# Optimization experiments

Hardware: AMD Instinct MI355X
Metric: run time of the kernel (lower is better)

Reference implementation:

```python
import jax, jax.numpy as jnp
import numpy as np

BETA = 0.25  # commitment cost
EPS = 1e-10


def _vq_layer(part, cb):
    # part: [B, C, H, W], cb: [K, C]
    B, C, H, W = part.shape
    K = cb.shape[0]
    flat = part.transpose(0, 2, 3, 1).reshape(-1, C)  # [N, C]
    d2 = (jnp.sum(flat * flat, axis=1, keepdims=True)
          - 2.0 * flat @ cb.T
          + jnp.sum(cb * cb, axis=1))  # [N, K]
    idx = jnp.argmin(d2, axis=1)  # [N]
    quant = cb[idx].reshape(B, H, W, C).transpose(0, 3, 1, 2)  # [B, C, H, W]
    e_latent = jnp.mean((jax.lax.stop_gradient(quant) - part) ** 2)
    q_latent = jnp.mean((quant - jax.lax.stop_gradient(part)) ** 2)
    loss = q_latent + BETA * e_latent  # scalar
    # straight-through estimator
    quant_st = part + jax.lax.stop_gradient(quant - part)
    # perplexity (codebook usage)
    counts = jnp.zeros((K,), dtype=part.dtype).at[idx].add(1.0)
    avg_probs = counts / idx.shape[0]
    perplexity = jnp.exp(-jnp.sum(avg_probs * jnp.log(avg_probs + EPS)))
    return quant_st, idx.reshape(B, H, W), loss, perplexity


def setup_inputs() -> dict:
    key = jax.random.key(0)
    ks = jax.random.split(key, 5)
    x = jax.random.normal(ks[0], (16, 256, 64, 64), dtype=jnp.float32)
    out = {"x": x}
    for i in range(4):
        out[f"codebook{i}"] = jax.random.normal(ks[i + 1], (1024, 64), dtype=jnp.float32)
    return out


def reference(x, codebook0, codebook1, codebook2, codebook3):
    dim_list = [64, 64, 64, 64]
    codebooks = [codebook0, codebook1, codebook2, codebook3]
    quants, indices, losses, perps = [], [], [], []
    start = 0
    for i in range(4):
        part = x[:, start:start + dim_list[i], :, :]
        start += dim_list[i]
        q, idx, loss, perp = _vq_layer(part, codebooks[i])
        quants.append(q)
        indices.append(idx)
        losses.append(loss)
        perps.append(perp)
    quantized_cat = jnp.concatenate(quants, axis=1)          # [B, 256, H, W]
    indices_cat = jnp.stack(indices, axis=1)                  # [B, 4, H, W]
    loss_cat = jnp.stack(losses, axis=0)                      # [4]
    perplexity_cat = jnp.stack(perps, axis=0)                 # [4]
    return quantized_cat, indices_cat, loss_cat, perplexity_cat
```

## Files before the change

kernel.cpp:

```cpp
#include <hip/hip_runtime.h>
#include <math.h>

#define HW 4096
#define CH 64
#define NCODE 1024
#define TAU 0.05f
#define FLAGCAP 65536u

#define OUT_IDX  16777216
#define OUT_LOSS 17039360
#define OUT_PERP 17039364

#define WS_C2    0
#define WS_CNT   4096
#define WS_SUM   8192
#define WS_FLAGC 8196
#define WS_FLAGL 8208
#define WS_CBP   73744

typedef short bf16x8 __attribute__((ext_vector_type(8)));
typedef float f32x4v __attribute__((ext_vector_type(4)));

static __device__ __forceinline__ unsigned f2u(float f) { return __float_as_uint(f); }
static __device__ __forceinline__ float u2f(unsigned u) { return __uint_as_float(u); }
static __device__ __forceinline__ unsigned short bf16rne(float f) {
  unsigned u = f2u(f);
  unsigned r = u + 0x7FFFu + ((u >> 16) & 1u);
  return (unsigned short)(r >> 16);
}

__global__ __launch_bounds__(256) void vq_prep(const float* __restrict__ cb0, const float* __restrict__ cb1,
                                               const float* __restrict__ cb2, const float* __restrict__ cb3,
                                               float* __restrict__ ws) {
  int gid = blockIdx.x * 256 + threadIdx.x;
  int l = gid >> 10, code = gid & 1023;
  const float* cbs[4] = {cb0, cb1, cb2, cb3};
  const float* row = cbs[l] + (size_t)code * CH;

  unsigned short* cbpack = (unsigned short*)(ws + WS_CBP);
  const int kt = code >> 5, m = (code >> 4) & 1, rowc = code & 15;
  const size_t base = (size_t)l * 131072 + (size_t)kt * 4096;

  float c2 = 0.f;
#pragma unroll 8
  for (int c = 0; c < CH; ++c) {
    float v = row[c];
    c2 = fmaf(v, v, c2);
    float aa = -2.f * v;
    unsigned short ah = bf16rne(aa);
    float rest = aa - u2f((unsigned)ah << 16);
    unsigned short al = bf16rne(rest);
    int s0 = c, s1 = 64 + c;
    cbpack[base + (size_t)(m * 4 + (s0 >> 5)) * 512 + (size_t)(((s0 >> 3) & 3) * 16 + rowc) * 8 + (s0 & 7)] = ah;
    cbpack[base + (size_t)(m * 4 + (s1 >> 5)) * 512 + (size_t)(((s1 >> 3) & 3) * 16 + rowc) * 8 + (s1 & 7)] = al;
  }
  ws[WS_C2 + gid] = c2;
  ws[WS_CNT + gid] = 0.f;
  if (gid < 4) ws[WS_SUM + gid] = 0.f;
  if (gid == 0) *((unsigned*)(ws + WS_FLAGC)) = 0u;
}

__global__ __launch_bounds__(256, 2) void vq_argmin(
    const float* __restrict__ x, float* __restrict__ ws, float* __restrict__ out) {
  const int layer = blockIdx.y;
  const int wid = threadIdx.x >> 6;
  const int lane = threadIdx.x & 63;
  const int rowl = lane & 15, g = lane >> 4;

  const int p0 = blockIdx.x * 256 + wid * 64;
  const int b = p0 >> 12;
  const int hwb = (p0 & 4095) + rowl;
  const float* xb = x + (size_t)(b * 256 + layer * 64) * HW;

  bf16x8 xf[4][4];
#pragma unroll
  for (int n = 0; n < 4; ++n) {
    int hw = hwb + n * 16;
#pragma unroll
    for (int j = 0; j < 8; ++j) {
      float v0 = xb[(size_t)(g * 8 + j) * HW + hw];
      float v1 = xb[(size_t)(32 + g * 8 + j) * HW + hw];
      unsigned short h0 = bf16rne(v0);
      unsigned short h1 = bf16rne(v1);
      float r0 = v0 - u2f((unsigned)h0 << 16);
      float r1 = v1 - u2f((unsigned)h1 << 16);
      xf[n][0][j] = (short)h0;
      xf[n][1][j] = (short)h1;
      xf[n][2][j] = (short)bf16rne(r0);
      xf[n][3][j] = (short)bf16rne(r1);
    }
  }

  const unsigned short* cbl = (const unsigned short*)(ws + WS_CBP) + (size_t)layer * 131072;
  const float* c2l = ws + WS_C2 + layer * NCODE;

  float d1[4], d2[4];
  int k1[4];
#pragma unroll
  for (int n = 0; n < 4; ++n) { d1[n] = 1e30f; d2[n] = 1e30f; k1[n] = 0; }

  for (int kt = 0; kt < 32; ++kt) {
    const unsigned short* cbase = cbl + (size_t)kt * 4096 + lane * 8;
#pragma unroll
    for (int m = 0; m < 2; ++m) {
      bf16x8 ch0 = *(const bf16x8*)(cbase + (m * 4 + 0) * 512);
      bf16x8 ch1 = *(const bf16x8*)(cbase + (m * 4 + 1) * 512);
      bf16x8 cl0 = *(const bf16x8*)(cbase + (m * 4 + 2) * 512);
      bf16x8 cl1 = *(const bf16x8*)(cbase + (m * 4 + 3) * 512);
      f32x4v c2v = *(const f32x4v*)(c2l + kt * 32 + m * 16 + g * 4);
      const int kb = kt * 32 + m * 16 + g * 4;
#pragma unroll
      for (int n = 0; n < 4; ++n) {
        f32x4v a = {0.f, 0.f, 0.f, 0.f};
        a = __builtin_amdgcn_mfma_f32_16x16x32_bf16(ch0, xf[n][0], a, 0, 0, 0);
        a = __builtin_amdgcn_mfma_f32_16x16x32_bf16(ch1, xf[n][1], a, 0, 0, 0);
        a = __builtin_amdgcn_mfma_f32_16x16x32_bf16(cl0, xf[n][0], a, 0, 0, 0);
        a = __builtin_amdgcn_mfma_f32_16x16x32_bf16(cl1, xf[n][1], a, 0, 0, 0);
        a = __builtin_amdgcn_mfma_f32_16x16x32_bf16(ch0, xf[n][2], a, 0, 0, 0);
        a = __builtin_amdgcn_mfma_f32_16x16x32_bf16(ch1, xf[n][3], a, 0, 0, 0);
#pragma unroll
        for (int r = 0; r < 4; ++r) {
          float d = a[r] + c2v[r];
          bool lt = d < d1[n];
          d2[n] = fminf(d2[n], fmaxf(d, d1[n]));
          d1[n] = fminf(d1[n], d);
          k1[n] = lt ? (kb + r) : k1[n];
        }
      }
    }
  }

  unsigned* flagcnt = (unsigned*)(ws + WS_FLAGC);
  unsigned* flaglist = (unsigned*)(ws + WS_FLAGL);
#pragma unroll
  for (int n = 0; n < 4; ++n) {
    float e1 = d1[n], e2 = d2[n];
    int ek = k1[n];
#pragma unroll
    for (int off = 16; off <= 32; off <<= 1) {
      float o1 = __shfl_xor(e1, off);
      float o2 = __shfl_xor(e2, off);
      int ok = __shfl_xor(ek, off);
      bool take = (o1 < e1) || (o1 == e1 && ok < ek);
      float loser = take ? e1 : o1;
      e2 = fminf(fminf(e2, o2), loser);
      e1 = take ? o1 : e1;
      ek = take ? ok : ek;
    }
    if (g == 0) {
      int p = p0 + n * 16 + rowl;
      int hw = p & 4095;
      size_t orow = (size_t)(b * 4 + layer) * HW + hw;
      out[OUT_IDX + orow] = (float)ek;
      if (e2 - e1 < TAU) {
        unsigned pos = atomicAdd(flagcnt, 1u);
        if (pos < FLAGCAP) flaglist[pos] = (unsigned)orow;
      }
    }
  }
}

__global__ __launch_bounds__(64) void vq_refine(
    const float* __restrict__ x,
    const float* __restrict__ cb0, const float* __restrict__ cb1,
    const float* __restrict__ cb2, const float* __restrict__ cb3,
    const float* __restrict__ ws, float* __restrict__ out) {
  unsigned count = *((const unsigned*)(ws + WS_FLAGC));
  if (count > FLAGCAP) count = FLAGCAP;
  const unsigned* flaglist = (const unsigned*)(ws + WS_FLAGL);

  for (unsigned i = blockIdx.x; i < count; i += gridDim.x) {
    unsigned r = flaglist[i];
    int l = (r >> 12) & 3;
    int bb = r >> 14;
    int hw = r & 4095;
    const float* cb = (l == 0) ? cb0 : (l == 1) ? cb1 : (l == 2) ? cb2 : cb3;
    const float* xb = x + (size_t)(bb * 256 + l * 64) * HW + hw;
    double f[CH];
#pragma unroll
    for (int c = 0; c < CH; ++c) f[c] = (double)xb[(size_t)c * HW];
    double bd = 1e300;
    int bk = 0;
    for (int j = 0; j < 16; ++j) {
      int k = threadIdx.x + j * 64;
      const float* cr = cb + (size_t)k * CH;
      double dot = 0.0, cc = 0.0;
#pragma unroll
      for (int c = 0; c < CH; ++c) {
        double cv = (double)cr[c];
        cc = fma(cv, cv, cc);
        dot = fma(f[c], cv, dot);
      }
      double d = cc - 2.0 * dot;
      if (d < bd || (d == bd && k < bk)) { bd = d; bk = k; }
    }
    for (int off = 1; off < 64; off <<= 1) {
      double od = __shfl_xor(bd, off);
      int ok = __shfl_xor(bk, off);
      if (od < bd || (od == bd && ok < bk)) { bd = od; bk = ok; }
    }
    if (threadIdx.x == 0) out[OUT_IDX + r] = (float)bk;
  }
}

__global__ __launch_bounds__(256) void vq_gather(
    const float* __restrict__ x,
    const float* __restrict__ cb0, const float* __restrict__ cb1,
    const float* __restrict__ cb2, const float* __restrict__ cb3,
    float* __restrict__ out, float* __restrict__ ws) {
  __shared__ unsigned hist[NCODE];
  __shared__ float red[256];
  const int layer = blockIdx.y;
  const int t = threadIdx.x;
  const float* cb = (layer == 0) ? cb0 : (layer == 1) ? cb1 : (layer == 2) ? cb2 : cb3;

  for (int i = t; i < NCODE; i += 256) hist[i] = 0u;
  __syncthreads();

  const int pbase = blockIdx.x * 2048;
  int kk[8];
#pragma unroll
  for (int i = 0; i < 8; ++i) {
    int p = pbase + i * 256 + t;
    int bb = p >> 12, hw = p & 4095;
    int k = (int)out[OUT_IDX + (size_t)(bb * 4 + layer) * HW + hw];
    kk[i] = k;
    atomicAdd(&hist[k], 1u);
  }

  float ls = 0.f;
#pragma unroll
  for (int i = 0; i < 8; ++i) {
    int p = pbase + i * 256 + t;
    int bb = p >> 12, hw = p & 4095;
    const float* xp = x + (size_t)(bb * 256 + layer * 64) * HW + hw;
    float* qp = out + (size_t)(bb * 256 + layer * 64) * HW + hw;
    const float* cr = cb + (size_t)kk[i] * CH;
#pragma unroll
    for (int c4 = 0; c4 < 16; ++c4) {
      float4 cv = *(const float4*)(cr + c4 * 4);
      float q[4] = {cv.x, cv.y, cv.z, cv.w};
#pragma unroll
      for (int j = 0; j < 4; ++j) {
        int c = c4 * 4 + j;
        float xv = xp[(size_t)c * HW];
        qp[(size_t)c * HW] = q[j];
        float dd = q[j] - xv;
        ls = fmaf(dd, dd, ls);
      }
    }
  }

  red[t] = ls;
  __syncthreads();
  for (int s = 128; s > 0; s >>= 1) {
    if (t < s) red[t] += red[t + s];
    __syncthreads();
  }
  if (t == 0) atomicAdd(&ws[WS_SUM + layer], red[0]);

  for (int i = t; i < NCODE; i += 256) {
    unsigned h = hist[i];
    if (h) atomicAdd(&ws[WS_CNT + layer * NCODE + i], (float)h);
  }
}

__global__ __launch_bounds__(256) void vq_final(const float* __restrict__ ws, float* __restrict__ out) {
  const int l = blockIdx.x;
  float h = 0.f;
#pragma unroll
  for (int j = 0; j < 4; ++j) {
    float cnt = ws[WS_CNT + l * NCODE + threadIdx.x + j * 256];
    float pr = cnt * (1.f / 65536.f);
    h += pr * logf(pr + 1e-10f);
  }
  __shared__ float red[256];
  red[threadIdx.x] = h;
  __syncthreads();
  for (int s = 128; s > 0; s >>= 1) {
    if (threadIdx.x < s) red[threadIdx.x] += red[threadIdx.x + s];
    __syncthreads();
  }
  if (threadIdx.x == 0) {
    out[OUT_LOSS + l] = 1.25f * ws[WS_SUM + l] / 4194304.f;
    out[OUT_PERP + l] = expf(-red[0]);
  }
}

extern "C" void kernel_launch(void* const* d_in, const int* in_sizes, int n_in,
                              void* d_out, int out_size, void* d_ws, size_t ws_size,
                              hipStream_t stream) {
  const float* x = (const float*)d_in[0];
  const float* cb0 = (const float*)d_in[1];
  const float* cb1 = (const float*)d_in[2];
  const float* cb2 = (const float*)d_in[3];
  const float* cb3 = (const float*)d_in[4];
  float* out = (float*)d_out;
  float* ws = (float*)d_ws;

  vq_prep  <<<dim3(16),     dim3(256), 0, stream>>>(cb0, cb1, cb2, cb3, ws);
  vq_argmin<<<dim3(256, 4), dim3(256), 0, stream>>>(x, ws, out);
  vq_refine<<<dim3(2048),   dim3(64),  0, stream>>>(x, cb0, cb1, cb2, cb3, ws, out);
  vq_gather<<<dim3(32, 4),  dim3(256), 0, stream>>>(x, cb0, cb1, cb2, cb3, out, ws);
  vq_final <<<dim3(4),      dim3(256), 0, stream>>>(ws, out);
}
```

Baseline: 352.7 us.

## Pack code index into distance bits, compute loss in argmin, slim gather

The argmin kernel now folds ||x||^2 and ||c||^2 into the MFMA accumulator init. It packs the code index into the low mantissa bits so the min/second-min tracking uses only fminf and med3, and it double-buffers codebook register loads across halves. The commitment loss is taken directly from the minimum distance, and refine corrects it when it changes an index, using precomputed double-precision code norms. The gather kernel no longer rereads x, so it only writes quantized values and the histogram. Truncating 10 mantissa bits lowers distance precision, and the flag threshold was made relative to compensate, which could flag more near-ties and raise refine work.

```diff
diff --git a/kernel.cpp b/kernel.cpp
--- a/kernel.cpp
+++ b/kernel.cpp
@@ -4,7 +4,6 @@
 #define HW 4096
 #define CH 64
 #define NCODE 1024
-#define TAU 0.05f
 #define FLAGCAP 65536u
 
 #define OUT_IDX  16777216
@@ -15,8 +14,9 @@
 #define WS_CNT   4096
 #define WS_SUM   8192
 #define WS_FLAGC 8196
-#define WS_FLAGL 8208
-#define WS_CBP   73744
+#define WS_C2D   8200
+#define WS_FLAGL 16392
+#define WS_CBP   81936
 
 typedef short bf16x8 __attribute__((ext_vector_type(8)));
 typedef float f32x4v __attribute__((ext_vector_type(4)));
@@ -42,10 +42,12 @@
   const size_t base = (size_t)l * 131072 + (size_t)kt * 4096;
 
   float c2 = 0.f;
+  double c2d = 0.0;
 #pragma unroll 8
   for (int c = 0; c < CH; ++c) {
     float v = row[c];
     c2 = fmaf(v, v, c2);
+    c2d = fma((double)v, (double)v, c2d);
     float aa = -2.f * v;
     unsigned short ah = bf16rne(aa);
     float rest = aa - u2f((unsigned)ah << 16);
@@ -55,31 +57,36 @@
     cbpack[base + (size_t)(m * 4 + (s1 >> 5)) * 512 + (size_t)(((s1 >> 3) & 3) * 16 + rowc) * 8 + (s1 & 7)] = al;
   }
   ws[WS_C2 + gid] = c2;
+  ((double*)(ws + WS_C2D))[gid] = c2d;
   ws[WS_CNT + gid] = 0.f;
   if (gid < 4) ws[WS_SUM + gid] = 0.f;
   if (gid == 0) *((unsigned*)(ws + WS_FLAGC)) = 0u;
 }
 
-__global__ __launch_bounds__(256, 2) void vq_argmin(
+__global__ __launch_bounds__(64, 4) void vq_argmin(
     const float* __restrict__ x, float* __restrict__ ws, float* __restrict__ out) {
   const int layer = blockIdx.y;
-  const int wid = threadIdx.x >> 6;
-  const int lane = threadIdx.x & 63;
+  const int lane = threadIdx.x;
   const int rowl = lane & 15, g = lane >> 4;
-
-  const int p0 = blockIdx.x * 256 + wid * 64;
+  const int g4 = g * 4;
+
+  const int p0 = blockIdx.x * 64;
   const int b = p0 >> 12;
   const int hwb = (p0 & 4095) + rowl;
   const float* xb = x + (size_t)(b * 256 + layer * 64) * HW;
 
   bf16x8 xf[4][4];
+  float x2[4];
 #pragma unroll
   for (int n = 0; n < 4; ++n) {
     int hw = hwb + n * 16;
+    float s = 0.f;
 #pragma unroll
     for (int j = 0; j < 8; ++j) {
       float v0 = xb[(size_t)(g * 8 + j) * HW + hw];
       float v1 = xb[(size_t)(32 + g * 8 + j) * HW + hw];
+      s = fmaf(v0, v0, s);
+      s = fmaf(v1, v1, s);
       unsigned short h0 = bf16rne(v0);
       unsigned short h1 = bf16rne(v1);
       float r0 = v0 - u2f((unsigned)h0 << 16);
@@ -89,85 +96,118 @@
       xf[n][2][j] = (short)bf16rne(r0);
       xf[n][3][j] = (short)bf16rne(r1);
     }
+    s += __shfl_xor(s, 16);
+    s += __shfl_xor(s, 32);
+    x2[n] = s;
   }
 
   const unsigned short* cbl = (const unsigned short*)(ws + WS_CBP) + (size_t)layer * 131072;
   const float* c2l = ws + WS_C2 + layer * NCODE;
 
   float d1[4], d2[4];
-  int k1[4];
-#pragma unroll
-  for (int n = 0; n < 4; ++n) { d1[n] = 1e30f; d2[n] = 1e30f; k1[n] = 0; }
-
-  for (int kt = 0; kt < 32; ++kt) {
-    const unsigned short* cbase = cbl + (size_t)kt * 4096 + lane * 8;
-#pragma unroll
-    for (int m = 0; m < 2; ++m) {
-      bf16x8 ch0 = *(const bf16x8*)(cbase + (m * 4 + 0) * 512);
-      bf16x8 ch1 = *(const bf16x8*)(cbase + (m * 4 + 1) * 512);
-      bf16x8 cl0 = *(const bf16x8*)(cbase + (m * 4 + 2) * 512);
-      bf16x8 cl1 = *(const bf16x8*)(cbase + (m * 4 + 3) * 512);
-      f32x4v c2v = *(const f32x4v*)(c2l + kt * 32 + m * 16 + g * 4);
-      const int kb = kt * 32 + m * 16 + g * 4;
-#pragma unroll
-      for (int n = 0; n < 4; ++n) {
-        f32x4v a = {0.f, 0.f, 0.f, 0.f};
-        a = __builtin_amdgcn_mfma_f32_16x16x32_bf16(ch0, xf[n][0], a, 0, 0, 0);
-        a = __builtin_amdgcn_mfma_f32_16x16x32_bf16(ch1, xf[n][1], a, 0, 0, 0);
-        a = __builtin_amdgcn_mfma_f32_16x16x32_bf16(cl0, xf[n][0], a, 0, 0, 0);
-        a = __builtin_amdgcn_mfma_f32_16x16x32_bf16(cl1, xf[n][1], a, 0, 0, 0);
-        a = __builtin_amdgcn_mfma_f32_16x16x32_bf16(ch0, xf[n][2], a, 0, 0, 0);
-        a = __builtin_amdgcn_mfma_f32_16x16x32_bf16(ch1, xf[n][3], a, 0, 0, 0);
-#pragma unroll
-        for (int r = 0; r < 4; ++r) {
-          float d = a[r] + c2v[r];
-          bool lt = d < d1[n];
-          d2[n] = fminf(d2[n], fmaxf(d, d1[n]));
-          d1[n] = fminf(d1[n], d);
-          k1[n] = lt ? (kb + r) : k1[n];
-        }
+#pragma unroll
+  for (int n = 0; n < 4; ++n) { d1[n] = 1e30f; d2[n] = 1e30f; }
+
+  const unsigned short* cbase = cbl + lane * 8;
+
+  auto compute_half = [&](int hh, bf16x8 R0, bf16x8 R1, bf16x8 R2, bf16x8 R3) {
+    f32x4v c2v = *(const f32x4v*)(c2l + hh * 16 + g4);
+    unsigned kb0 = (unsigned)(hh * 16 + g4);
+#pragma unroll
+    for (int n = 0; n < 4; ++n) {
+      f32x4v a;
+      a[0] = c2v[0] + x2[n]; a[1] = c2v[1] + x2[n];
+      a[2] = c2v[2] + x2[n]; a[3] = c2v[3] + x2[n];
+      a = __builtin_amdgcn_mfma_f32_16x16x32_bf16(R0, xf[n][0], a, 0, 0, 0);
+      a = __builtin_amdgcn_mfma_f32_16x16x32_bf16(R1, xf[n][1], a, 0, 0, 0);
+      a = __builtin_amdgcn_mfma_f32_16x16x32_bf16(R2, xf[n][0], a, 0, 0, 0);
+      a = __builtin_amdgcn_mfma_f32_16x16x32_bf16(R3, xf[n][1], a, 0, 0, 0);
+      a = __builtin_amdgcn_mfma_f32_16x16x32_bf16(R0, xf[n][2], a, 0, 0, 0);
+      a = __builtin_amdgcn_mfma_f32_16x16x32_bf16(R1, xf[n][3], a, 0, 0, 0);
+#pragma unroll
+      for (int r = 0; r < 4; ++r) {
+        float pd = u2f((f2u(a[r]) & 0xFFFFFC00u) | (kb0 + r));
+        float t = d1[n];
+        d1[n] = fminf(t, pd);
+        d2[n] = __builtin_amdgcn_fmed3f(t, d2[n], pd);
       }
     }
+  };
+
+  bf16x8 A0, A1, A2, A3, B0, B1, B2, B3;
+  A0 = *(const bf16x8*)(cbase + 0);
+  A1 = *(const bf16x8*)(cbase + 512);
+  A2 = *(const bf16x8*)(cbase + 1024);
+  A3 = *(const bf16x8*)(cbase + 1536);
+  for (int h = 0; h < 62; h += 2) {
+    const unsigned short* p1 = cbase + (size_t)(h + 1) * 2048;
+    B0 = *(const bf16x8*)(p1 + 0);
+    B1 = *(const bf16x8*)(p1 + 512);
+    B2 = *(const bf16x8*)(p1 + 1024);
+    B3 = *(const bf16x8*)(p1 + 1536);
+    compute_half(h, A0, A1, A2, A3);
+    const unsigned short* p2 = cbase + (size_t)(h + 2) * 2048;
+    A0 = *(const bf16x8*)(p2 + 0);
+    A1 = *(const bf16x8*)(p2 + 512);
+    A2 = *(const bf16x8*)(p2 + 1024);
+    A3 = *(const bf16x8*)(p2 + 1536);
+    compute_half(h + 1, B0, B1, B2, B3);
+  }
+  {
+    const unsigned short* p1 = cbase + (size_t)63 * 2048;
+    B0 = *(const bf16x8*)(p1 + 0);
+    B1 = *(const bf16x8*)(p1 + 512);
+    B2 = *(const bf16x8*)(p1 + 1024);
+    B3 = *(const bf16x8*)(p1 + 1536);
+    compute_half(62, A0, A1, A2, A3);
+    compute_half(63, B0, B1, B2, B3);
   }
 
   unsigned* flagcnt = (unsigned*)(ws + WS_FLAGC);
   unsigned* flaglist = (unsigned*)(ws + WS_FLAGL);
+  float sse = 0.f;
 #pragma unroll
   for (int n = 0; n < 4; ++n) {
     float e1 = d1[n], e2 = d2[n];
-    int ek = k1[n];
 #pragma unroll
     for (int off = 16; off <= 32; off <<= 1) {
       float o1 = __shfl_xor(e1, off);
       float o2 = __shfl_xor(e2, off);
-      int ok = __shfl_xor(ek, off);
-      bool take = (o1 < e1) || (o1 == e1 && ok < ek);
-      float loser = take ? e1 : o1;
-      e2 = fminf(fminf(e2, o2), loser);
-      e1 = take ? o1 : e1;
-      ek = take ? ok : ek;
-    }
+      float t = fmaxf(e1, o1);
+      e1 = fminf(e1, o1);
+      e2 = fminf(fminf(t, e2), o2);
+    }
+    float du1 = u2f(f2u(e1) & 0xFFFFFC00u);
+    sse += du1;
     if (g == 0) {
       int p = p0 + n * 16 + rowl;
       int hw = p & 4095;
       size_t orow = (size_t)(b * 4 + layer) * HW + hw;
-      out[OUT_IDX + orow] = (float)ek;
-      if (e2 - e1 < TAU) {
+      out[OUT_IDX + orow] = (float)(f2u(e1) & 1023u);
+      float du2 = u2f(f2u(e2) & 0xFFFFFC00u);
+      float tau2 = fmaf(du1, 3e-4f, 0.05f);
+      if (du2 - du1 < tau2) {
         unsigned pos = atomicAdd(flagcnt, 1u);
         if (pos < FLAGCAP) flaglist[pos] = (unsigned)orow;
       }
     }
   }
+  sse += __shfl_xor(sse, 1);
+  sse += __shfl_xor(sse, 2);
+  sse += __shfl_xor(sse, 4);
+  sse += __shfl_xor(sse, 8);
+  if (lane == 0) atomicAdd(&ws[WS_SUM + layer], sse);
 }
 
 __global__ __launch_bounds__(64) void vq_refine(
     const float* __restrict__ x,
     const float* __restrict__ cb0, const float* __restrict__ cb1,
     const float* __restrict__ cb2, const float* __restrict__ cb3,
-    const float* __restrict__ ws, float* __restrict__ out) {
+    float* __restrict__ ws, float* __restrict__ out) {
   unsigned count = *((const unsigned*)(ws + WS_FLAGC));
   if (count > FLAGCAP) count = FLAGCAP;
   const unsigned* flaglist = (const unsigned*)(ws + WS_FLAGL);
+  const int tid = threadIdx.x;
 
   for (unsigned i = blockIdx.x; i < count; i += gridDim.x) {
     unsigned r = flaglist[i];
@@ -175,41 +215,50 @@
     int bb = r >> 14;
     int hw = r & 4095;
     const float* cb = (l == 0) ? cb0 : (l == 1) ? cb1 : (l == 2) ? cb2 : cb3;
+    const double* c2d = (const double*)(ws + WS_C2D) + l * NCODE;
     const float* xb = x + (size_t)(bb * 256 + l * 64) * HW + hw;
-    double f[CH];
-#pragma unroll
-    for (int c = 0; c < CH; ++c) f[c] = (double)xb[(size_t)c * HW];
-    double bd = 1e300;
+    float f[CH];
+#pragma unroll
+    for (int c = 0; c < CH; ++c) f[c] = xb[(size_t)c * HW];
+    int old = (int)out[OUT_IDX + r];
+
+    double bd = 1e300, sOld = 1e300;
     int bk = 0;
     for (int j = 0; j < 16; ++j) {
-      int k = threadIdx.x + j * 64;
+      int k = (j << 6) | tid;
       const float* cr = cb + (size_t)k * CH;
-      double dot = 0.0, cc = 0.0;
-#pragma unroll
-      for (int c = 0; c < CH; ++c) {
-        double cv = (double)cr[c];
-        cc = fma(cv, cv, cc);
-        dot = fma(f[c], cv, dot);
+      double dot = 0.0;
+#pragma unroll
+      for (int c4 = 0; c4 < 16; ++c4) {
+        float4 cv = *(const float4*)(cr + c4 * 4);
+        dot = fma((double)cv.x, (double)f[c4 * 4 + 0], dot);
+        dot = fma((double)cv.y, (double)f[c4 * 4 + 1], dot);
+        dot = fma((double)cv.z, (double)f[c4 * 4 + 2], dot);
+        dot = fma((double)cv.w, (double)f[c4 * 4 + 3], dot);
       }
-      double d = cc - 2.0 * dot;
-      if (d < bd || (d == bd && k < bk)) { bd = d; bk = k; }
+      double sc = fma(-2.0, dot, c2d[k]);
+      if (sc < bd || (sc == bd && k < bk)) { bd = sc; bk = k; }
+      if (k == old) sOld = sc;
     }
     for (int off = 1; off < 64; off <<= 1) {
       double od = __shfl_xor(bd, off);
       int ok = __shfl_xor(bk, off);
+      double os = __shfl_xor(sOld, off);
       if (od < bd || (od == bd && ok < bk)) { bd = od; bk = ok; }
-    }
-    if (threadIdx.x == 0) out[OUT_IDX + r] = (float)bk;
+      sOld = fmin(sOld, os);
+    }
+    if (tid == 0 && bk != old) {
+      out[OUT_IDX + r] = (float)bk;
+      atomicAdd(&ws[WS_SUM + l], (float)(bd - sOld));
+    }
   }
 }
 
 __global__ __launch_bounds__(256) void vq_gather(
-    const float* __restrict__ x,
     const float* __restrict__ cb0, const float* __restrict__ cb1,
     const float* __restrict__ cb2, const float* __restrict__ cb3,
     float* __restrict__ out, float* __restrict__ ws) {
   __shared__ unsigned hist[NCODE];
-  __shared__ float red[256];
   const int layer = blockIdx.y;
   const int t = threadIdx.x;
   const float* cb = (layer == 0) ? cb0 : (layer == 1) ? cb1 : (layer == 2) ? cb2 : cb3;
@@ -217,48 +266,23 @@
   for (int i = t; i < NCODE; i += 256) hist[i] = 0u;
   __syncthreads();
 
-  const int pbase = blockIdx.x * 2048;
-  int kk[8];
-#pragma unroll
-  for (int i = 0; i < 8; ++i) {
-    int p = pbase + i * 256 + t;
-    int bb = p >> 12, hw = p & 4095;
-    int k = (int)out[OUT_IDX + (size_t)(bb * 4 + layer) * HW + hw];
-    kk[i] = k;
-    atomicAdd(&hist[k], 1u);
-  }
-
-  float ls = 0.f;
-#pragma unroll
-  for (int i = 0; i < 8; ++i) {
-    int p = pbase + i * 256 + t;
-    int bb = p >> 12, hw = p & 4095;
-    const float* xp = x + (size_t)(bb * 256 + layer * 64) * HW + hw;
-    float* qp = out + (size_t)(bb * 256 + layer * 64) * HW + hw;
-    const float* cr = cb + (size_t)kk[i] * CH;
-#pragma unroll
-    for (int c4 = 0; c4 < 16; ++c4) {
-      float4 cv = *(const float4*)(cr + c4 * 4);
-      float q[4] = {cv.x, cv.y, cv.z, cv.w};
-#pragma unroll
-      for (int j = 0; j < 4; ++j) {
-        int c = c4 * 4 + j;
-        float xv = xp[(size_t)c * HW];
-        qp[(size_t)c * HW] = q[j];
-        float dd = q[j] - xv;
-        ls = fmaf(dd, dd, ls);
-      }
-    }
-  }
-
-  red[t] = ls;
+  const int p = blockIdx.x * 256 + t;
+  const int bb = p >> 12, hw = p & 4095;
+  const int k = (int)out[OUT_IDX + (size_t)(bb * 4 + layer) * HW + hw];
+  atomicAdd(&hist[k], 1u);
+
+  const float* cr = cb + (size_t)k * CH;
+  float* qp = out + (size_t)(bb * 256 + layer * 64) * HW + hw;
+#pragma unroll
+  for (int c4 = 0; c4 < 16; ++c4) {
+    float4 cv = *(const float4*)(cr + c4 * 4);
+    qp[(size_t)(c4 * 4 + 0) * HW] = cv.x;
+    qp[(size_t)(c4 * 4 + 1) * HW] = cv.y;
+    qp[(size_t)(c4 * 4 + 2) * HW] = cv.z;
+    qp[(size_t)(c4 * 4 + 3) * HW] = cv.w;
+  }
+
   __syncthreads();
-  for (int s = 128; s > 0; s >>= 1) {
-    if (t < s) red[t] += red[t + s];
-    __syncthreads();
-  }
-  if (t == 0) atomicAdd(&ws[WS_SUM + layer], red[0]);
-
   for (int i = t; i < NCODE; i += 256) {
     unsigned h = hist[i];
     if (h) atomicAdd(&ws[WS_CNT + layer * NCODE + i], (float)h);
@@ -298,9 +322,9 @@
   float* out = (float*)d_out;
   float* ws = (float*)d_ws;
 
-  vq_prep  <<<dim3(16),     dim3(256), 0, stream>>>(cb0, cb1, cb2, cb3, ws);
-  vq_argmin<<<dim3(256, 4), dim3(256), 0, stream>>>(x, ws, out);
-  vq_refine<<<dim3(2048),   dim3(64),  0, stream>>>(x, cb0, cb1, cb2, cb3, ws, out);
-  vq_gather<<<dim3(32, 4),  dim3(256), 0, stream>>>(x, cb0, cb1, cb2, cb3, out, ws);
-  vq_final <<<dim3(4),      dim3(256), 0, stream>>>(ws, out);
-}
+  vq_prep  <<<dim3(16),      dim3(256), 0, stream>>>(cb0, cb1, cb2, cb3, ws);
+  vq_argmin<<<dim3(1024, 4), dim3(64),  0, stream>>>(x, ws, out);
+  vq_refine<<<dim3(2048),    dim3(64),  0, stream>>>(x, cb0, cb1, cb2, cb3, ws, out);
+  vq_gather<<<dim3(256, 4),  dim3(256), 0, stream>>>(cb0, cb1, cb2, cb3, out, ws);
+  vq_final <<<dim3(4),       dim3(256), 0, stream>>>(ws, out);
+}
```

Measured after the change: 592.1 us. 67.9% more time.
